# Kernel optimization log

Hardware: AMD Instinct MI355X
Metric: run time of the kernel (lower is better)

The kernel has to match this reference:

```python
import jax, jax.numpy as jnp
import numpy as np

DIM = 768
HEADS = 12


def setup_inputs() -> dict:
    key = jax.random.key(0)
    k1, k2, k3, k4 = jax.random.split(key, 4)
    x = jax.random.normal(k1, (8, 1024, DIM), dtype=jnp.float32)
    # qkv: Linear(dim, 3*dim, bias=False); torch stores weight as (out, in), y = x @ W.T
    w_qkv = jax.random.normal(k2, (3 * DIM, DIM), dtype=jnp.float32) * (DIM ** -0.5)
    w_fc = jax.random.normal(k3, (DIM, DIM), dtype=jnp.float32) * (DIM ** -0.5)
    b_fc = jax.random.normal(k4, (DIM,), dtype=jnp.float32) * 0.02
    return {"x": x, "w_qkv": w_qkv, "w_fc": w_fc, "b_fc": b_fc}


def reference(x, w_qkv, w_fc, b_fc):
    b, n, dim = x.shape
    h = HEADS
    d = dim // h
    qkv = jnp.einsum('bnd,ed->bne', x, w_qkv)  # [b, n, 3*dim]
    q, k, v = jnp.split(qkv, 3, axis=-1)
    # b n (h d) -> b h n d
    q = q.reshape(b, n, h, d).transpose(0, 2, 1, 3)
    k = k.reshape(b, n, h, d).transpose(0, 2, 1, 3)
    v = v.reshape(b, n, h, d).transpose(0, 2, 1, 3)
    # NOTE: original module computes d_k = dim**-0.5 but never applies it.
    scores = jnp.einsum('bhqd,bhkd->bhqk', q, k)  # unscaled, faithful to source
    attn = jax.nn.softmax(scores, axis=-1)
    out = jnp.einsum('bhqk,bhkd->bhqd', attn, v)
    out = out.transpose(0, 2, 1, 3).reshape(b, n, dim)  # b h n d -> b n (h d)
    out = jnp.einsum('bnd,ed->bne', out, w_fc) + b_fc
    return out
```

## Files before the change

kernel.cpp:

```cpp
#include <hip/hip_runtime.h>
#include <cstdint>
#include <cstddef>

typedef __bf16 bf16;
typedef __bf16 bf16x4 __attribute__((ext_vector_type(4)));
typedef __bf16 bf16x8 __attribute__((ext_vector_type(8)));
typedef float f32x4 __attribute__((ext_vector_type(4)));
typedef float f32x16 __attribute__((ext_vector_type(16)));

typedef const __attribute__((address_space(1))) void* gas_ptr;
typedef __attribute__((address_space(3))) void* las_ptr;

#define GLOAD_LDS16(g, l) __builtin_amdgcn_global_load_lds((gas_ptr)(g), (las_ptr)(l), 16, 0, 0)

__global__ void cvt_f32_bf16(const float* __restrict__ in, bf16* __restrict__ out, int n4) {
  int i = blockIdx.x * blockDim.x + threadIdx.x;
  int stride = gridDim.x * blockDim.x;
  for (; i < n4; i += stride) {
    float4 v = reinterpret_cast<const float4*>(in)[i];
    bf16x4 o;
    o[0] = (bf16)v.x; o[1] = (bf16)v.y; o[2] = (bf16)v.z; o[3] = (bf16)v.w;
    reinterpret_cast<bf16x4*>(out)[i] = o;
  }
}

template <int MODE>
__global__ __launch_bounds__(256, 3) void gemm_bt(
    const bf16* __restrict__ A, const bf16* __restrict__ B,
    int M, int N, int K,
    bf16* __restrict__ outb, float* __restrict__ outf,
    const float* __restrict__ bias) {
  constexpr int BK = 32;
  __shared__ bf16 ldsA[2][4096];
  __shared__ bf16 ldsB[2][4096];
  const int tid = threadIdx.x;
  const int l = tid & 63;
  const int w = tid >> 6;
  const int wr = w >> 1, wc = w & 1;
  const int lr = l & 15, lg = l >> 4;

  const int gx = gridDim.x, nwg = gx * gridDim.y;
  int bid = blockIdx.y * gx + blockIdx.x;
  bid = (bid & 7) * (nwg >> 3) + (bid >> 3);
  const int brow = (bid % gx) * 128;
  const int bcol = (bid / gx) * 128;

  const bf16* sa0 = A + (size_t)(brow + w * 16 + lr) * K + lg * 8;
  const bf16* sa1 = sa0 + (size_t)64 * K;
  const bf16* sb0 = B + (size_t)(bcol + w * 16 + lr) * K + lg * 8;
  const bf16* sb1 = sb0 + (size_t)64 * K;
  const int d0 = w * 512 + l * 8;
  const int d1 = (4 + w) * 512 + l * 8;

  f32x4 acc[4][4] = {};

  GLOAD_LDS16(sa0, &ldsA[0][d0]);
  GLOAD_LDS16(sa1, &ldsA[0][d1]);
  GLOAD_LDS16(sb0, &ldsB[0][d0]);
  GLOAD_LDS16(sb1, &ldsB[0][d1]);
  asm volatile("s_waitcnt vmcnt(0)" ::: "memory");
  __syncthreads();

  int p = 0;
  for (int k0 = 0; k0 < K; k0 += BK) {
    if (k0 + BK < K) {
      GLOAD_LDS16(sa0 + (k0 + BK), &ldsA[p ^ 1][d0]);
      GLOAD_LDS16(sa1 + (k0 + BK), &ldsA[p ^ 1][d1]);
      GLOAD_LDS16(sb0 + (k0 + BK), &ldsB[p ^ 1][d0]);
      GLOAD_LDS16(sb1 + (k0 + BK), &ldsB[p ^ 1][d1]);
    }
    bf16x8 af[4], bfr[4];
#pragma unroll
    for (int mi = 0; mi < 4; mi++)
      af[mi] = *reinterpret_cast<const bf16x8*>(&ldsA[p][(wr * 4 + mi) * 512 + l * 8]);
#pragma unroll
    for (int ni = 0; ni < 4; ni++)
      bfr[ni] = *reinterpret_cast<const bf16x8*>(&ldsB[p][(wc * 4 + ni) * 512 + l * 8]);
#pragma unroll
    for (int mi = 0; mi < 4; mi++)
#pragma unroll
      for (int ni = 0; ni < 4; ni++)
        acc[mi][ni] = __builtin_amdgcn_mfma_f32_16x16x32_bf16(af[mi], bfr[ni], acc[mi][ni], 0, 0, 0);
    asm volatile("s_waitcnt vmcnt(0)" ::: "memory");
    __syncthreads();
    p ^= 1;
  }

#pragma unroll
  for (int mi = 0; mi < 4; mi++) {
#pragma unroll
    for (int r = 0; r < 4; r++) {
      const int m = brow + wr * 64 + mi * 16 + lg * 4 + r;
#pragma unroll
      for (int ni = 0; ni < 4; ni++) {
        const int e = bcol + wc * 64 + ni * 16 + lr;
        const float v = acc[mi][ni][r];
        if (MODE == 1) {
          outf[(size_t)m * N + e] = v + bias[e];
        } else {
          outb[(size_t)m * N + e] = (bf16)v;
        }
      }
    }
  }
}

__global__ __launch_bounds__(256) void vtrans(const bf16* __restrict__ qkv,
                                              bf16* __restrict__ vtb) {
  __shared__ bf16 t[64 * 72];
  const int bh = blockIdx.x;
  const int b = bh / 12, h = bh % 12;
  const int nt = blockIdx.y;
  const int tid = threadIdx.x;
#pragma unroll
  for (int it = 0; it < 2; it++) {
    const int item = tid + it * 256;
    const int nl = item >> 3, c = item & 7;
    bf16x8 v = *reinterpret_cast<const bf16x8*>(
        &qkv[(size_t)(b * 1024 + nt * 64 + nl) * 2304 + 1536 + h * 64 + c * 8]);
#pragma unroll
    for (int j = 0; j < 8; j++) t[(c * 8 + j) * 72 + nl] = v[j];
  }
  __syncthreads();
#pragma unroll
  for (int it = 0; it < 2; it++) {
    const int item = tid + it * 256;
    const int d = item >> 3, c2 = item & 7;
    bf16x8 v = *reinterpret_cast<const bf16x8*>(&t[d * 72 + c2 * 8]);
    *reinterpret_cast<bf16x8*>(
        &vtb[(size_t)bh * 65536 + d * 1024 + nt * 64 + c2 * 8]) = v;
  }
}

__global__ __launch_bounds__(256, 3) void attn_kernel(
    const bf16* __restrict__ QKV, const bf16* __restrict__ Vt,
    bf16* __restrict__ Out) {
  __shared__ bf16 Kb[2][4096];
  __shared__ bf16 Vb[2][4096];
  const int tid = threadIdx.x;
  const int l = tid & 63;
  const int w = tid >> 6;
  const int ql = l & 31;
  const int hi = l >> 5;
  const int bh = blockIdx.x;
  const int b = bh / 12, h = bh % 12;
  const int q0 = blockIdx.y * 128 + w * 32;
  const bf16* Vh = Vt + (size_t)bh * 65536;
  constexpr float L2E = 1.4426950408889634f;

  const int kdst0 = (0 * 4 + w) * 512 + l * 8;
  const int kdst1 = (1 * 4 + w) * 512 + l * 8;
  const bf16* ksrc0 = QKV + (size_t)(b * 1024 + ql) * 2304 + 768 + h * 64 + w * 16 + hi * 8;
  const bf16* ksrc1 = ksrc0 + (size_t)32 * 2304;
  const bf16* vsrc0 = Vh + (size_t)((w & 1) * 32 + ql) * 1024 + ((0 * 4 + w) >> 1) * 16 + hi * 8;
  const bf16* vsrc1 = Vh + (size_t)((w & 1) * 32 + ql) * 1024 + ((1 * 4 + w) >> 1) * 16 + hi * 8;

  const bf16* Qrow = QKV + (size_t)(b * 1024 + q0 + ql) * 2304 + h * 64;
  bf16x8 qf[4];
#pragma unroll
  for (int s = 0; s < 4; s++)
    qf[s] = *reinterpret_cast<const bf16x8*>(&Qrow[s * 16 + hi * 8]);

  f32x16 o[2] = {};
  float ls0 = 0.f, ls1 = 0.f, ls2 = 0.f, ls3 = 0.f;

  GLOAD_LDS16(ksrc0, &Kb[0][kdst0]);
  GLOAD_LDS16(ksrc1, &Kb[0][kdst1]);
  GLOAD_LDS16(vsrc0, &Vb[0][kdst0]);
  GLOAD_LDS16(vsrc1, &Vb[0][kdst1]);
  asm volatile("s_waitcnt vmcnt(0)" ::: "memory");
  __syncthreads();

  int p = 0;
  for (int it = 0; it < 16; ++it) {
    const int kt = it * 64;
    if (it < 15) {
      GLOAD_LDS16(ksrc0 + (size_t)(kt + 64) * 2304, &Kb[p ^ 1][kdst0]);
      GLOAD_LDS16(ksrc1 + (size_t)(kt + 64) * 2304, &Kb[p ^ 1][kdst1]);
      GLOAD_LDS16(vsrc0 + (kt + 64), &Vb[p ^ 1][kdst0]);
      GLOAD_LDS16(vsrc1 + (kt + 64), &Vb[p ^ 1][kdst1]);
    }

    bf16x8 kf[8];
#pragma unroll
    for (int r = 0; r < 8; r++)
      kf[r] = *reinterpret_cast<const bf16x8*>(&Kb[p][r * 512 + l * 8]);
    f32x16 st0 = {}, st1 = {};
    __builtin_amdgcn_s_setprio(1);
#pragma unroll
    for (int s = 0; s < 4; s++) {
      st0 = __builtin_amdgcn_mfma_f32_32x32x16_bf16(kf[s], qf[s], st0, 0, 0, 0);
      st1 = __builtin_amdgcn_mfma_f32_32x32x16_bf16(kf[4 + s], qf[s], st1, 0, 0, 0);
    }
    __builtin_amdgcn_s_setprio(0);

#pragma unroll
    for (int r = 0; r < 16; r++) {
      float a0 = st0[r] * L2E, a1 = st1[r] * L2E;
      float e0, e1;
      asm("v_exp_f32 %0, %1" : "=v"(e0) : "v"(a0));
      asm("v_exp_f32 %0, %1" : "=v"(e1) : "v"(a1));
      st0[r] = e0; st1[r] = e1;
    }
#pragma unroll
    for (int r = 0; r < 16; r += 2) {
      ls0 += st0[r]; ls1 += st0[r + 1];
      ls2 += st1[r]; ls3 += st1[r + 1];
    }

    bf16x8 pfv[4];
#pragma unroll
    for (int t = 0; t < 4; t++) {
      const int c8 = (t & 1) * 8;
      const f32x16& sv = (t < 2) ? st0 : st1;
      uint32_t wA0, wA1, wB0, wB1;
      asm("v_cvt_pk_bf16_f32 %0, %1, %2" : "=v"(wA0) : "v"(sv[c8 + 0]), "v"(sv[c8 + 1]));
      asm("v_cvt_pk_bf16_f32 %0, %1, %2" : "=v"(wA1) : "v"(sv[c8 + 2]), "v"(sv[c8 + 3]));
      asm("v_cvt_pk_bf16_f32 %0, %1, %2" : "=v"(wB0) : "v"(sv[c8 + 4]), "v"(sv[c8 + 5]));
      asm("v_cvt_pk_bf16_f32 %0, %1, %2" : "=v"(wB1) : "v"(sv[c8 + 6]), "v"(sv[c8 + 7]));
      asm("v_permlane32_swap_b32 %0, %1" : "+v"(wA0), "+v"(wB0));
      asm("v_permlane32_swap_b32 %0, %1" : "+v"(wA1), "+v"(wB1));
      union { uint32_t u[4]; bf16x8 v; } pf;
      pf.u[0] = wA0; pf.u[1] = wA1; pf.u[2] = wB0; pf.u[3] = wB1;
      pfv[t] = pf.v;
    }

    bf16x8 vf[8];
#pragma unroll
    for (int r = 0; r < 8; r++)
      vf[r] = *reinterpret_cast<const bf16x8*>(&Vb[p][r * 512 + l * 8]);
    __builtin_amdgcn_s_setprio(1);
#pragma unroll
    for (int t = 0; t < 4; t++) {
      o[0] = __builtin_amdgcn_mfma_f32_32x32x16_bf16(vf[t * 2 + 0], pfv[t], o[0], 0, 0, 0);
      o[1] = __builtin_amdgcn_mfma_f32_32x32x16_bf16(vf[t * 2 + 1], pfv[t], o[1], 0, 0, 0);
    }
    __builtin_amdgcn_s_setprio(0);

    asm volatile("s_waitcnt vmcnt(0)" ::: "memory");
    __syncthreads();
    p ^= 1;
  }

  float lsum = (ls0 + ls1) + (ls2 + ls3);
  lsum += __shfl_xor(lsum, 32);
  const float rl = 1.0f / lsum;
  bf16* orow = Out + (size_t)(b * 1024 + q0 + ql) * 768 + h * 64;
#pragma unroll
  for (int dh = 0; dh < 2; dh++)
#pragma unroll
    for (int rq = 0; rq < 4; rq++) {
      union { ushort us[4]; uint2 v; } pk;
#pragma unroll
      for (int i = 0; i < 4; i++) {
        const bf16 hv = (bf16)(o[dh][rq * 4 + i] * rl);
        pk.us[i] = __builtin_bit_cast(ushort, hv);
      }
      *reinterpret_cast<uint2*>(&orow[dh * 32 + rq * 8 + hi * 4]) = pk.v;
    }
}

extern "C" void kernel_launch(void* const* d_in, const int* in_sizes, int n_in,
                              void* d_out, int out_size, void* d_ws, size_t ws_size,
                              hipStream_t stream) {
  const float* x = (const float*)d_in[0];
  const float* w_qkv = (const float*)d_in[1];
  const float* w_fc = (const float*)d_in[2];
  const float* b_fc = (const float*)d_in[3];
  float* out = (float*)d_out;
  char* ws = (char*)d_ws;

  bf16* xb = (bf16*)(ws);
  bf16* vtb = (bf16*)(ws);
  bf16* wqkb = (bf16*)(ws + 12582912);
  bf16* wfcb = (bf16*)(ws + 16121856);
  bf16* qkvb = (bf16*)(ws + 17301504);
  bf16* aob = (bf16*)(ws + 55050240);

  cvt_f32_bf16<<<2048, 256, 0, stream>>>(x, xb, 6291456 / 4);
  cvt_f32_bf16<<<1728, 256, 0, stream>>>(w_qkv, wqkb, 1769472 / 4);
  cvt_f32_bf16<<<576, 256, 0, stream>>>(w_fc, wfcb, 589824 / 4);

  gemm_bt<0><<<dim3(64, 18), 256, 0, stream>>>(xb, wqkb, 8192, 2304, 768,
                                               qkvb, nullptr, nullptr);

  vtrans<<<dim3(96, 16), 256, 0, stream>>>(qkvb, vtb);

  attn_kernel<<<dim3(96, 8), 256, 0, stream>>>(qkvb, vtb, aob);

  gemm_bt<1><<<dim3(64, 6), 256, 0, stream>>>(aob, wfcb, 8192, 768, 768,
                                              nullptr, out, b_fc);
}
```

Before: 159.5 us.

## Triple-buffer GEMM LDS pipeline with two-stage prefetch and XCD-aware tile mapping

Moves the GEMM main loop from double to triple LDS buffering, keeping two K-tiles of global-to-LDS loads in flight and waiting with vmcnt(4) instead of draining to zero each iteration. The block-to-tile mapping now gives each XCD a contiguous range of row tiles so neighbouring blocks share A rows in cache, and MFMA sections run at raised wave priority. Costs are more LDS per block, which can lower occupancy under launch_bounds(256,3), and redundant clamped loads in the last iterations. The new mapping assumes gx is a multiple of 8 and that gx/8 is a power of two.

```diff
diff --git a/kernel.cpp b/kernel.cpp
--- a/kernel.cpp
+++ b/kernel.cpp
@@ -31,19 +31,19 @@
     bf16* __restrict__ outb, float* __restrict__ outf,
     const float* __restrict__ bias) {
   constexpr int BK = 32;
-  __shared__ bf16 ldsA[2][4096];
-  __shared__ bf16 ldsB[2][4096];
+  __shared__ bf16 ldsA[3][4096];
+  __shared__ bf16 ldsB[3][4096];
   const int tid = threadIdx.x;
   const int l = tid & 63;
   const int w = tid >> 6;
   const int wr = w >> 1, wc = w & 1;
   const int lr = l & 15, lg = l >> 4;
 
-  const int gx = gridDim.x, nwg = gx * gridDim.y;
-  int bid = blockIdx.y * gx + blockIdx.x;
-  bid = (bid & 7) * (nwg >> 3) + (bid >> 3);
-  const int brow = (bid % gx) * 128;
-  const int bcol = (bid / gx) * 128;
+  const int gx = gridDim.x;
+  const int bid = blockIdx.y * gx + blockIdx.x;
+  const int xcd = bid & 7, c = bid >> 3, rpx = gx >> 3;
+  const int brow = (xcd * rpx + (c & (rpx - 1))) * 128;
+  const int bcol = (c / rpx) * 128;
 
   const bf16* sa0 = A + (size_t)(brow + w * 16 + lr) * K + lg * 8;
   const bf16* sa1 = sa0 + (size_t)64 * K;
@@ -58,17 +58,24 @@
   GLOAD_LDS16(sa1, &ldsA[0][d1]);
   GLOAD_LDS16(sb0, &ldsB[0][d0]);
   GLOAD_LDS16(sb1, &ldsB[0][d1]);
-  asm volatile("s_waitcnt vmcnt(0)" ::: "memory");
-  __syncthreads();
+  GLOAD_LDS16(sa0 + BK, &ldsA[1][d0]);
+  GLOAD_LDS16(sa1 + BK, &ldsA[1][d1]);
+  GLOAD_LDS16(sb0 + BK, &ldsB[1][d0]);
+  GLOAD_LDS16(sb1 + BK, &ldsB[1][d1]);
 
   int p = 0;
   for (int k0 = 0; k0 < K; k0 += BK) {
-    if (k0 + BK < K) {
-      GLOAD_LDS16(sa0 + (k0 + BK), &ldsA[p ^ 1][d0]);
-      GLOAD_LDS16(sa1 + (k0 + BK), &ldsA[p ^ 1][d1]);
-      GLOAD_LDS16(sb0 + (k0 + BK), &ldsB[p ^ 1][d0]);
-      GLOAD_LDS16(sb1 + (k0 + BK), &ldsB[p ^ 1][d1]);
-    }
+    asm volatile("s_waitcnt vmcnt(4)" ::: "memory");
+    __syncthreads();
+
+    int kn = k0 + 2 * BK;
+    if (kn >= K) kn = k0;
+    const int pt = (p >= 1) ? p - 1 : 2;
+    GLOAD_LDS16(sa0 + kn, &ldsA[pt][d0]);
+    GLOAD_LDS16(sa1 + kn, &ldsA[pt][d1]);
+    GLOAD_LDS16(sb0 + kn, &ldsB[pt][d0]);
+    GLOAD_LDS16(sb1 + kn, &ldsB[pt][d1]);
+
     bf16x8 af[4], bfr[4];
 #pragma unroll
     for (int mi = 0; mi < 4; mi++)
@@ -76,14 +83,14 @@
 #pragma unroll
     for (int ni = 0; ni < 4; ni++)
       bfr[ni] = *reinterpret_cast<const bf16x8*>(&ldsB[p][(wc * 4 + ni) * 512 + l * 8]);
+    __builtin_amdgcn_s_setprio(1);
 #pragma unroll
     for (int mi = 0; mi < 4; mi++)
 #pragma unroll
       for (int ni = 0; ni < 4; ni++)
         acc[mi][ni] = __builtin_amdgcn_mfma_f32_16x16x32_bf16(af[mi], bfr[ni], acc[mi][ni], 0, 0, 0);
-    asm volatile("s_waitcnt vmcnt(0)" ::: "memory");
-    __syncthreads();
-    p ^= 1;
+    __builtin_amdgcn_s_setprio(0);
+    p = (p == 2) ? 0 : p + 1;
   }
 
 #pragma unroll
```

Result: no change. 156.4 us (-1.9%).

## Single-buffer GEMM LDS, raise occupancy, remap blocks by XCD

Applied to the files above, without the earlier changes.

Drops LDS double buffering in the GEMM so each tile is loaded, waited on and synced before compute, and raises launch bounds from 3 to 4 waves per SIMD. It also replaces the block swizzle with an XCD-aware mapping that gives each XCD a group of eight consecutive row tiles. The aim is to rely on extra resident blocks rather than in-block prefetch to hide latency, and to improve L2 reuse per XCD. The cost is that loads no longer overlap MFMA work within a block. The new mapping hardcodes 8 row groups per XCD, which assumes a specific grid shape.

```diff
diff --git a/kernel.cpp b/kernel.cpp
--- a/kernel.cpp
+++ b/kernel.cpp
@@ -25,25 +25,24 @@
 }
 
 template <int MODE>
-__global__ __launch_bounds__(256, 3) void gemm_bt(
+__global__ __launch_bounds__(256, 4) void gemm_bt(
     const bf16* __restrict__ A, const bf16* __restrict__ B,
     int M, int N, int K,
     bf16* __restrict__ outb, float* __restrict__ outf,
     const float* __restrict__ bias) {
   constexpr int BK = 32;
-  __shared__ bf16 ldsA[2][4096];
-  __shared__ bf16 ldsB[2][4096];
+  __shared__ bf16 ldsA[4096];
+  __shared__ bf16 ldsB[4096];
   const int tid = threadIdx.x;
   const int l = tid & 63;
   const int w = tid >> 6;
   const int wr = w >> 1, wc = w & 1;
   const int lr = l & 15, lg = l >> 4;
 
-  const int gx = gridDim.x, nwg = gx * gridDim.y;
-  int bid = blockIdx.y * gx + blockIdx.x;
-  bid = (bid & 7) * (nwg >> 3) + (bid >> 3);
-  const int brow = (bid % gx) * 128;
-  const int bcol = (bid / gx) * 128;
+  const int bid = blockIdx.y * gridDim.x + blockIdx.x;
+  const int xcd = bid & 7, c = bid >> 3;
+  const int brow = (xcd * 8 + (c & 7)) * 128;
+  const int bcol = (c >> 3) * 128;
 
   const bf16* sa0 = A + (size_t)(brow + w * 16 + lr) * K + lg * 8;
   const bf16* sa1 = sa0 + (size_t)64 * K;
@@ -54,36 +53,27 @@
 
   f32x4 acc[4][4] = {};
 
-  GLOAD_LDS16(sa0, &ldsA[0][d0]);
-  GLOAD_LDS16(sa1, &ldsA[0][d1]);
-  GLOAD_LDS16(sb0, &ldsB[0][d0]);
-  GLOAD_LDS16(sb1, &ldsB[0][d1]);
-  asm volatile("s_waitcnt vmcnt(0)" ::: "memory");
-  __syncthreads();
-
-  int p = 0;
   for (int k0 = 0; k0 < K; k0 += BK) {
-    if (k0 + BK < K) {
-      GLOAD_LDS16(sa0 + (k0 + BK), &ldsA[p ^ 1][d0]);
-      GLOAD_LDS16(sa1 + (k0 + BK), &ldsA[p ^ 1][d1]);
-      GLOAD_LDS16(sb0 + (k0 + BK), &ldsB[p ^ 1][d0]);
-      GLOAD_LDS16(sb1 + (k0 + BK), &ldsB[p ^ 1][d1]);
-    }
+    GLOAD_LDS16(sa0 + k0, &ldsA[d0]);
+    GLOAD_LDS16(sa1 + k0, &ldsA[d1]);
+    GLOAD_LDS16(sb0 + k0, &ldsB[d0]);
+    GLOAD_LDS16(sb1 + k0, &ldsB[d1]);
+    asm volatile("s_waitcnt vmcnt(0)" ::: "memory");
+    __syncthreads();
+
     bf16x8 af[4], bfr[4];
 #pragma unroll
     for (int mi = 0; mi < 4; mi++)
-      af[mi] = *reinterpret_cast<const bf16x8*>(&ldsA[p][(wr * 4 + mi) * 512 + l * 8]);
+      af[mi] = *reinterpret_cast<const bf16x8*>(&ldsA[(wr * 4 + mi) * 512 + l * 8]);
 #pragma unroll
     for (int ni = 0; ni < 4; ni++)
-      bfr[ni] = *reinterpret_cast<const bf16x8*>(&ldsB[p][(wc * 4 + ni) * 512 + l * 8]);
+      bfr[ni] = *reinterpret_cast<const bf16x8*>(&ldsB[(wc * 4 + ni) * 512 + l * 8]);
 #pragma unroll
     for (int mi = 0; mi < 4; mi++)
 #pragma unroll
       for (int ni = 0; ni < 4; ni++)
         acc[mi][ni] = __builtin_amdgcn_mfma_f32_16x16x32_bf16(af[mi], bfr[ni], acc[mi][ni], 0, 0, 0);
-    asm volatile("s_waitcnt vmcnt(0)" ::: "memory");
     __syncthreads();
-    p ^= 1;
   }
 
 #pragma unroll
```

Result: faster. 153.0 us (-4.0%).
